# Performance work log

Measured on AMD Instinct MI355X. Metric: run time of the kernel, lower is better.

Reference implementation:

```python
import jax, jax.numpy as jnp
import numpy as np

B, T, D = 2, 2048, 1024
H = 16
HD = D // H  # 64


def setup_inputs() -> dict:
    key = jax.random.key(0)
    k1, k2, k3, k4, k5 = jax.random.split(key, 5)
    s = 0.02
    return {
        "x": jax.random.normal(k1, (B, T, D), dtype=jnp.float32),
        "Wqkv": jax.random.normal(k2, (D, 3 * D), dtype=jnp.float32) * s,
        "bqkv": jax.random.normal(k3, (3 * D,), dtype=jnp.float32) * s,
        "Wout": jax.random.normal(k4, (D, D), dtype=jnp.float32) * s,
        "bout": jax.random.normal(k5, (D,), dtype=jnp.float32) * s,
    }


def reference(x, Wqkv, bqkv, Wout, bout):
    b, t, c = x.shape
    qkv = (x @ Wqkv + bqkv).reshape(b, t, 3, H, HD)
    q = jnp.transpose(qkv[:, :, 0], (0, 2, 1, 3))  # [B,H,T,HD]
    k = jnp.transpose(qkv[:, :, 1], (0, 2, 1, 3))
    v = jnp.transpose(qkv[:, :, 2], (0, 2, 1, 3))
    att = jnp.einsum("bhqd,bhkd->bhqk", q, k) * (HD ** -0.5)
    mask = jnp.tril(jnp.ones((t, t), dtype=bool))  # causal, no past kv
    att = jnp.where(mask, att, -jnp.inf)
    att = jax.nn.softmax(att, axis=-1)
    y = jnp.einsum("bhqk,bhkd->bhqd", att, v)
    y = jnp.transpose(y, (0, 2, 1, 3)).reshape(b, t, c)
    return y @ Wout + bout
```

## Files before the change

### kernel.cpp

```cpp
#include <hip/hip_runtime.h>
#include <hip/hip_bf16.h>
#include <math.h>

#define B_  2
#define T_  2048
#define D_  1024
#define H_  16
#define HD_ 64

typedef __attribute__((ext_vector_type(8))) short short8;
typedef __attribute__((ext_vector_type(4))) float f32x4;

#if __has_builtin(__builtin_amdgcn_exp2f)
#define EXP2F __builtin_amdgcn_exp2f
#else
#define EXP2F exp2f
#endif

__device__ __forceinline__ ushort f2bf(float x) {
    unsigned u = __builtin_bit_cast(unsigned, x);
    return (ushort)((u + 0x7FFFu + ((u >> 16) & 1u)) >> 16);
}

__device__ __forceinline__ unsigned pack_bf2_fast(float a, float b) {
    unsigned ua = __builtin_bit_cast(unsigned, a) + 0x8000u;
    unsigned ub = __builtin_bit_cast(unsigned, b) + 0x8000u;
    return (ua >> 16) | (ub & 0xFFFF0000u);
}

__device__ __forceinline__ void load_lds_16B(const ushort* g, ushort* l) {
    __builtin_amdgcn_global_load_lds(
        (const __attribute__((address_space(1))) unsigned*)g,
        (__attribute__((address_space(3))) unsigned*)l, 16, 0, 0);
}

__global__ __launch_bounds__(256)
void cast_x_kernel(const float* __restrict__ x, ushort* __restrict__ xb, int n4)
{
    int i = blockIdx.x * blockDim.x + threadIdx.x;
    for (; i < n4; i += gridDim.x * blockDim.x) {
        float4 v = ((const float4*)x)[i];
        ushort4 o = { f2bf(v.x), f2bf(v.y), f2bf(v.z), f2bf(v.w) };
        ((ushort4*)xb)[i] = o;
    }
}

__global__ __launch_bounds__(256)
void transpose_cast_w(const float* __restrict__ W, ushort* __restrict__ Wt,
                      int K, int M)
{
    __shared__ ushort Ts[64][65];
    const int m0 = blockIdx.x * 64, k0 = blockIdx.y * 64;
    const int tr = threadIdx.x >> 4;
    const int tc = threadIdx.x & 15;
    #pragma unroll
    for (int it = 0; it < 4; it++) {
        int k = tr + it * 16;
        float4 v = *(const float4*)&W[(size_t)(k0 + k) * M + m0 + tc * 4];
        Ts[tc * 4 + 0][k] = f2bf(v.x);
        Ts[tc * 4 + 1][k] = f2bf(v.y);
        Ts[tc * 4 + 2][k] = f2bf(v.z);
        Ts[tc * 4 + 3][k] = f2bf(v.w);
    }
    __syncthreads();
    const int mr = threadIdx.x >> 2;
    const int c4 = threadIdx.x & 3;
    #pragma unroll
    for (int it = 0; it < 4; it++) {
        int kk = c4 * 16 + it * 4;
        ushort4 o = { Ts[mr][kk], Ts[mr][kk + 1], Ts[mr][kk + 2], Ts[mr][kk + 3] };
        *(ushort4*)&Wt[(size_t)(m0 + mr) * K + k0 + kk] = o;
    }
}

template<int MODE>
__global__ __launch_bounds__(256)
void mfma_gemm(const ushort* __restrict__ A, const ushort* __restrict__ Bt,
               const float* __restrict__ bias, float* __restrict__ C,
               ushort* __restrict__ Qg, ushort* __restrict__ Kg,
               ushort* __restrict__ Vtg, int K, int M)
{
    __shared__ __align__(16) ushort lds[16384];
    ushort* Asl = lds;
    ushort* Bsl = lds + 8192;

    const int tid = threadIdx.x;
    const int w  = tid >> 6, L = tid & 63;
    const int lt = L & 15, lq = L >> 4;
    const int wr = w >> 1, wc = w & 1;
    const int m0 = blockIdx.x * 128, n0 = blockIdx.y * 128;
    const int rsub = L >> 3;
    const int pgr  = L & 7;

    f32x4 acc[4][4] = {};

    for (int k0 = 0; k0 < K; k0 += 64) {
        __syncthreads();
        #pragma unroll
        for (int j = 0; j < 4; j++) {
            const int row  = (w * 4 + j) * 8 + rsub;
            const int gran = pgr ^ rsub;
            load_lds_16B(A  + (size_t)(n0 + row) * K + k0 + gran * 8,
                         &Asl[row * 64 + pgr * 8]);
            load_lds_16B(Bt + (size_t)(m0 + row) * K + k0 + gran * 8,
                         &Bsl[row * 64 + pgr * 8]);
        }
        __syncthreads();

        #pragma unroll
        for (int ks = 0; ks < 2; ks++) {
            short8 af[4], bf[4];
            #pragma unroll
            for (int i = 0; i < 4; i++) {
                const int ra = wr * 64 + i * 16 + lt;
                af[i] = *(const short8*)&Asl[ra * 64 + (((ks * 4 + lq) ^ (ra & 7)) * 8)];
                const int rb = wc * 64 + i * 16 + lt;
                bf[i] = *(const short8*)&Bsl[rb * 64 + (((ks * 4 + lq) ^ (rb & 7)) * 8)];
            }
            #pragma unroll
            for (int i = 0; i < 4; i++)
                #pragma unroll
                for (int j = 0; j < 4; j++)
                    acc[i][j] = __builtin_amdgcn_mfma_f32_16x16x32_bf16(af[i], bf[j], acc[i][j], 0, 0, 0);
        }
    }

    if (MODE == 0) {
        #pragma unroll
        for (int j = 0; j < 4; j++) {
            const int m = m0 + wc * 64 + j * 16 + lt;
            const float bv = bias[m];
            #pragma unroll
            for (int i = 0; i < 4; i++) {
                const int n = n0 + wr * 64 + i * 16 + lq * 4;
                #pragma unroll
                for (int r = 0; r < 4; r++)
                    C[(size_t)(n + r) * M + m] = acc[i][j][r] + bv;
            }
        }
    } else {
        const int s = m0 >> 10;
        const float qs = (s == 0) ? 0.18033688011112042f : 1.0f;
        #pragma unroll
        for (int j = 0; j < 4; j++) {
            const int m = m0 + wc * 64 + j * 16 + lt;
            const float bv = bias[m];
            const int h = (m >> 6) & 15, d = m & 63;
            #pragma unroll
            for (int i = 0; i < 4; i++) {
                const int n = n0 + wr * 64 + i * 16 + lq * 4;
                const int b = n >> 11, t = n & 2047;
                if (s < 2) {
                    ushort* dst = (s == 0 ? Qg : Kg);
                    #pragma unroll
                    for (int r = 0; r < 4; r++)
                        dst[((size_t)(b * H_ + h) * T_ + t + r) * HD_ + d] =
                            f2bf((acc[i][j][r] + bv) * qs);
                } else {
                    ushort4 o = { f2bf(acc[i][j][0] + bv), f2bf(acc[i][j][1] + bv),
                                  f2bf(acc[i][j][2] + bv), f2bf(acc[i][j][3] + bv) };
                    *(ushort4*)&Vtg[((size_t)(b * H_ + h) * HD_ + d) * T_ + t] = o;
                }
            }
        }
    }
}

__global__ __launch_bounds__(256, 4)
void attn_mfma(const ushort* __restrict__ Qg, const ushort* __restrict__ Kg,
               const ushort* __restrict__ Vtg, ushort* __restrict__ yb)
{
    const int h = blockIdx.y, b = blockIdx.z;
    const int flip = ((blockIdx.y >> 3) ^ blockIdx.z) & 1;
    const int qb = flip ? blockIdx.x : (31 - blockIdx.x);
    const int tid = threadIdx.x;
    const int w  = tid >> 6, L = tid & 63;
    const int lt = L & 15, lq = L >> 4;
    const int kswz = lt & 7;

    __shared__ __align__(16) ushort Ks [128 * 64];
    __shared__ __align__(16) ushort Vts[64 * 128];
    __shared__ __align__(16) ushort Ps [4][16 * 40];

    const size_t bh = (size_t)(b * H_ + h);
    const ushort* Qbase  = Qg  + bh * T_ * HD_;
    const ushort* Kbase  = Kg  + bh * T_ * HD_;
    const ushort* Vtbase = Vtg + bh * HD_ * T_;

    const int q_glob = qb * 64 + w * 16 + lt;
    const short8 qf0 = *(const short8*)(Qbase + (size_t)q_glob * HD_ + lq * 8);
    const short8 qf1 = *(const short8*)(Qbase + (size_t)q_glob * HD_ + 32 + lq * 8);

    f32x4 acc_o[4] = {};
    float lsum = 0.f;

    const int krow = tid >> 3, kpg = tid & 7;
    const int vrow = tid >> 4, vpg = tid & 15;
    const int nk = (qb + 2) >> 1;

    for (int kb = 0; kb < nk; kb++) {
        __syncthreads();
        #pragma unroll
        for (int rr = 0; rr < 4; rr++) {
            const int row = krow + 32 * rr;
            load_lds_16B(Kbase + (size_t)(kb * 128 + row) * HD_ + (kpg ^ (row & 7)) * 8,
                         &Ks[row * 64 + kpg * 8]);
        }
        #pragma unroll
        for (int rr = 0; rr < 4; rr++) {
            const int d = vrow + 16 * rr;
            load_lds_16B(Vtbase + (size_t)d * T_ + kb * 128 + (vpg ^ (d & 7)) * 8,
                         &Vts[d * 128 + vpg * 8]);
        }
        __syncthreads();

        if (kb < nk - 1) {
            #pragma unroll
            for (int ks = 0; ks < 4; ks++) {
                const int row0 = (2 * ks) * 16 + lt;
                const int row1 = row0 + 16;
                short8 a00 = *(const short8*)&Ks[row0 * 64 + ((lq ^ kswz) * 8)];
                short8 a01 = *(const short8*)&Ks[row0 * 64 + (((4 + lq) ^ kswz) * 8)];
                short8 a10 = *(const short8*)&Ks[row1 * 64 + ((lq ^ kswz) * 8)];
                short8 a11 = *(const short8*)&Ks[row1 * 64 + (((4 + lq) ^ kswz) * 8)];
                f32x4 c0 = {}, c1 = {};
                c0 = __builtin_amdgcn_mfma_f32_16x16x32_bf16(a00, qf0, c0, 0, 0, 0);
                c0 = __builtin_amdgcn_mfma_f32_16x16x32_bf16(a01, qf1, c0, 0, 0, 0);
                c1 = __builtin_amdgcn_mfma_f32_16x16x32_bf16(a10, qf0, c1, 0, 0, 0);
                c1 = __builtin_amdgcn_mfma_f32_16x16x32_bf16(a11, qf1, c1, 0, 0, 0);

                float p0 = EXP2F(c0[0]), p1 = EXP2F(c0[1]);
                float p2 = EXP2F(c0[2]), p3 = EXP2F(c0[3]);
                float p4 = EXP2F(c1[0]), p5 = EXP2F(c1[1]);
                float p6 = EXP2F(c1[2]), p7 = EXP2F(c1[3]);
                lsum += ((p0 + p1) + (p2 + p3)) + ((p4 + p5) + (p6 + p7));
                uint2 pk0 = { pack_bf2_fast(p0, p1), pack_bf2_fast(p2, p3) };
                uint2 pk1 = { pack_bf2_fast(p4, p5), pack_bf2_fast(p6, p7) };
                *(uint2*)&Ps[w][lt * 40 + lq * 4]      = pk0;
                *(uint2*)&Ps[w][lt * 40 + 16 + lq * 4] = pk1;

                short8 pf = *(const short8*)&Ps[w][lt * 40 + lq * 8];

                #pragma unroll
                for (int dt = 0; dt < 4; dt++) {
                    const int vr = dt * 16 + lt;
                    short8 vf = *(const short8*)&Vts[vr * 128 + (((ks * 4 + lq) ^ kswz) * 8)];
                    acc_o[dt] = __builtin_amdgcn_mfma_f32_16x16x32_bf16(pf, vf, acc_o[dt], 0, 0, 0);
                }
            }
        } else {
            const int ksN = (qb & 1) ? 4 : 2;
            const int mk0 = (qb & 1) ? 2 : 0;
            for (int ks = 0; ks < ksN; ks++) {
                const int row0 = (2 * ks) * 16 + lt;
                const int row1 = row0 + 16;
                short8 a00 = *(const short8*)&Ks[row0 * 64 + ((lq ^ kswz) * 8)];
                short8 a01 = *(const short8*)&Ks[row0 * 64 + (((4 + lq) ^ kswz) * 8)];
                short8 a10 = *(const short8*)&Ks[row1 * 64 + ((lq ^ kswz) * 8)];
                short8 a11 = *(const short8*)&Ks[row1 * 64 + (((4 + lq) ^ kswz) * 8)];
                f32x4 c0 = {}, c1 = {};
                c0 = __builtin_amdgcn_mfma_f32_16x16x32_bf16(a00, qf0, c0, 0, 0, 0);
                c0 = __builtin_amdgcn_mfma_f32_16x16x32_bf16(a01, qf1, c0, 0, 0, 0);
                c1 = __builtin_amdgcn_mfma_f32_16x16x32_bf16(a10, qf0, c1, 0, 0, 0);
                c1 = __builtin_amdgcn_mfma_f32_16x16x32_bf16(a11, qf1, c1, 0, 0, 0);

                float p[8];
                #pragma unroll
                for (int r = 0; r < 4; r++) { p[r] = EXP2F(c0[r]); p[4 + r] = EXP2F(c1[r]); }
                if (ks >= mk0) {
                    const int key0 = kb * 128 + (2 * ks) * 16 + lq * 4;
                    #pragma unroll
                    for (int r = 0; r < 4; r++) {
                        if (key0 + r > q_glob)      p[r] = 0.f;
                        if (key0 + 16 + r > q_glob) p[4 + r] = 0.f;
                    }
                }
                lsum += ((p[0] + p[1]) + (p[2] + p[3])) + ((p[4] + p[5]) + (p[6] + p[7]));
                uint2 pk0 = { pack_bf2_fast(p[0], p[1]), pack_bf2_fast(p[2], p[3]) };
                uint2 pk1 = { pack_bf2_fast(p[4], p[5]), pack_bf2_fast(p[6], p[7]) };
                *(uint2*)&Ps[w][lt * 40 + lq * 4]      = pk0;
                *(uint2*)&Ps[w][lt * 40 + 16 + lq * 4] = pk1;

                short8 pf = *(const short8*)&Ps[w][lt * 40 + lq * 8];

                #pragma unroll
                for (int dt = 0; dt < 4; dt++) {
                    const int vr = dt * 16 + lt;
                    short8 vf = *(const short8*)&Vts[vr * 128 + (((ks * 4 + lq) ^ kswz) * 8)];
                    acc_o[dt] = __builtin_amdgcn_mfma_f32_16x16x32_bf16(pf, vf, acc_o[dt], 0, 0, 0);
                }
            }
        }
    }

    lsum += __shfl_xor(lsum, 16, 64);
    lsum += __shfl_xor(lsum, 32, 64);
    const float inv = 1.0f / lsum;

    float linv[4];
    #pragma unroll
    for (int r = 0; r < 4; r++) linv[r] = __shfl(inv, lq * 4 + r, 64);

    ushort* ybase = yb + (size_t)(b * T_ + qb * 64 + w * 16) * D_ + h * HD_;
    #pragma unroll
    for (int r = 0; r < 4; r++)
        #pragma unroll
        for (int dt = 0; dt < 4; dt++)
            ybase[(size_t)(lq * 4 + r) * D_ + dt * 16 + lt] = f2bf(acc_o[dt][r] * linv[r]);
}

extern "C" void kernel_launch(void* const* d_in, const int* in_sizes, int n_in,
                              void* d_out, int out_size, void* d_ws, size_t ws_size,
                              hipStream_t stream)
{
    const float* x    = (const float*)d_in[0];
    const float* Wqkv = (const float*)d_in[1];
    const float* bqkv = (const float*)d_in[2];
    const float* Wout = (const float*)d_in[3];
    const float* bout = (const float*)d_in[4];
    float* out = (float*)d_out;

    char* ws = (char*)d_ws;
    const size_t NT = (size_t)B_ * T_;
    ushort* xb     = (ushort*)ws;
    ushort* Wqkvt  = (ushort*)(ws + NT * D_ * 2);
    ushort* Woutt  = (ushort*)(ws + NT * D_ * 2 + (size_t)3 * D_ * D_ * 2);
    char*   p      = ws + NT * D_ * 2 + (size_t)4 * D_ * D_ * 2;
    const size_t qkv_elems = (size_t)B_ * H_ * T_ * HD_;
    ushort* Qg  = (ushort*)p;
    ushort* Kg  = (ushort*)(p + qkv_elems * 2);
    ushort* Vtg = (ushort*)(p + qkv_elems * 4);
    ushort* yb  = (ushort*)(p + qkv_elems * 6);

    cast_x_kernel<<<1024, 256, 0, stream>>>(x, xb, (int)(NT * D_ / 4));
    transpose_cast_w<<<dim3(3 * D_ / 64, D_ / 64), 256, 0, stream>>>(Wqkv, Wqkvt, D_, 3 * D_);
    transpose_cast_w<<<dim3(D_ / 64, D_ / 64), 256, 0, stream>>>(Wout, Woutt, D_, D_);

    mfma_gemm<1><<<dim3(3 * D_ / 128, NT / 128), 256, 0, stream>>>(
        xb, Wqkvt, bqkv, nullptr, Qg, Kg, Vtg, D_, 3 * D_);

    attn_mfma<<<dim3(32, H_, B_), 256, 0, stream>>>(Qg, Kg, Vtg, yb);

    mfma_gemm<0><<<dim3(D_ / 128, NT / 128), 256, 0, stream>>>(
        yb, Woutt, bout, out, nullptr, nullptr, nullptr, D_, D_);
}
```

Before: 180.2 us.

## Load attention K/V fragments directly from global and narrow out-projection GEMM tile

The attention kernel stops staging K and V^T tiles in shared memory behind block-wide barriers. Each wave now reads its MFMA operand fragments straight from global memory (relying on L2/cache reuse), and the main and last key blocks are merged into one loop with a masked tail. Separately, the GEMM is templated on its N tile width, and the output projection uses 64-wide tiles to double its block count for better CU occupancy. The risks are uncoalesced, redundant global loads per wave in attention, and less data reuse per block in the smaller GEMM tile.

```diff
diff --git a/kernel.cpp b/kernel.cpp
--- a/kernel.cpp
+++ b/kernel.cpp
@@ -73,14 +73,15 @@
     }
 }
 
-template<int MODE>
+template<int MODE, int BN>
 __global__ __launch_bounds__(256)
 void mfma_gemm(const ushort* __restrict__ A, const ushort* __restrict__ Bt,
                const float* __restrict__ bias, float* __restrict__ C,
                ushort* __restrict__ Qg, ushort* __restrict__ Kg,
                ushort* __restrict__ Vtg, int K, int M)
 {
-    __shared__ __align__(16) ushort lds[16384];
+    constexpr int JT = BN / 64;
+    __shared__ __align__(16) ushort lds[8192 + BN * 64];
     ushort* Asl = lds;
     ushort* Bsl = lds + 8192;
 
@@ -88,11 +89,11 @@
     const int w  = tid >> 6, L = tid & 63;
     const int lt = L & 15, lq = L >> 4;
     const int wr = w >> 1, wc = w & 1;
-    const int m0 = blockIdx.x * 128, n0 = blockIdx.y * 128;
+    const int m0 = blockIdx.x * BN, n0 = blockIdx.y * 128;
     const int rsub = L >> 3;
     const int pgr  = L & 7;
 
-    f32x4 acc[4][4] = {};
+    f32x4 acc[4][2 * JT] = {};
 
     for (int k0 = 0; k0 < K; k0 += 64) {
         __syncthreads();
@@ -100,8 +101,13 @@
         for (int j = 0; j < 4; j++) {
             const int row  = (w * 4 + j) * 8 + rsub;
             const int gran = pgr ^ rsub;
-            load_lds_16B(A  + (size_t)(n0 + row) * K + k0 + gran * 8,
+            load_lds_16B(A + (size_t)(n0 + row) * K + k0 + gran * 8,
                          &Asl[row * 64 + pgr * 8]);
+        }
+        #pragma unroll
+        for (int j = 0; j < BN / 32; j++) {
+            const int row  = (w * (BN / 32) + j) * 8 + rsub;
+            const int gran = pgr ^ rsub;
             load_lds_16B(Bt + (size_t)(m0 + row) * K + k0 + gran * 8,
                          &Bsl[row * 64 + pgr * 8]);
         }
@@ -109,26 +115,29 @@
 
         #pragma unroll
         for (int ks = 0; ks < 2; ks++) {
-            short8 af[4], bf[4];
+            short8 af[4], bf[2 * JT];
             #pragma unroll
             for (int i = 0; i < 4; i++) {
                 const int ra = wr * 64 + i * 16 + lt;
                 af[i] = *(const short8*)&Asl[ra * 64 + (((ks * 4 + lq) ^ (ra & 7)) * 8)];
-                const int rb = wc * 64 + i * 16 + lt;
-                bf[i] = *(const short8*)&Bsl[rb * 64 + (((ks * 4 + lq) ^ (rb & 7)) * 8)];
+            }
+            #pragma unroll
+            for (int j = 0; j < 2 * JT; j++) {
+                const int rb = wc * (BN / 2) + j * 16 + lt;
+                bf[j] = *(const short8*)&Bsl[rb * 64 + (((ks * 4 + lq) ^ (rb & 7)) * 8)];
             }
             #pragma unroll
             for (int i = 0; i < 4; i++)
                 #pragma unroll
-                for (int j = 0; j < 4; j++)
+                for (int j = 0; j < 2 * JT; j++)
                     acc[i][j] = __builtin_amdgcn_mfma_f32_16x16x32_bf16(af[i], bf[j], acc[i][j], 0, 0, 0);
         }
     }
 
     if (MODE == 0) {
         #pragma unroll
-        for (int j = 0; j < 4; j++) {
-            const int m = m0 + wc * 64 + j * 16 + lt;
+        for (int j = 0; j < 2 * JT; j++) {
+            const int m = m0 + wc * (BN / 2) + j * 16 + lt;
             const float bv = bias[m];
             #pragma unroll
             for (int i = 0; i < 4; i++) {
@@ -142,8 +151,8 @@
         const int s = m0 >> 10;
         const float qs = (s == 0) ? 0.18033688011112042f : 1.0f;
         #pragma unroll
-        for (int j = 0; j < 4; j++) {
-            const int m = m0 + wc * 64 + j * 16 + lt;
+        for (int j = 0; j < 2 * JT; j++) {
+            const int m = m0 + wc * (BN / 2) + j * 16 + lt;
             const float bv = bias[m];
             const int h = (m >> 6) & 15, d = m & 63;
             #pragma unroll
@@ -176,16 +185,13 @@
     const int tid = threadIdx.x;
     const int w  = tid >> 6, L = tid & 63;
     const int lt = L & 15, lq = L >> 4;
-    const int kswz = lt & 7;
-
-    __shared__ __align__(16) ushort Ks [128 * 64];
-    __shared__ __align__(16) ushort Vts[64 * 128];
-    __shared__ __align__(16) ushort Ps [4][16 * 40];
+
+    __shared__ __align__(16) ushort Ps[4][16 * 40];
 
     const size_t bh = (size_t)(b * H_ + h);
     const ushort* Qbase  = Qg  + bh * T_ * HD_;
-    const ushort* Kbase  = Kg  + bh * T_ * HD_;
-    const ushort* Vtbase = Vtg + bh * HD_ * T_;
+    const ushort* Kf     = Kg  + bh * T_ * HD_ + (size_t)lt * HD_ + lq * 8;
+    const ushort* Vf     = Vtg + bh * HD_ * T_ + (size_t)lt * T_  + lq * 8;
 
     const int q_glob = qb * 64 + w * 16 + lt;
     const short8 qf0 = *(const short8*)(Qbase + (size_t)q_glob * HD_ + lq * 8);
@@ -193,103 +199,55 @@
 
     f32x4 acc_o[4] = {};
     float lsum = 0.f;
-
-    const int krow = tid >> 3, kpg = tid & 7;
-    const int vrow = tid >> 4, vpg = tid & 15;
     const int nk = (qb + 2) >> 1;
 
     for (int kb = 0; kb < nk; kb++) {
-        __syncthreads();
-        #pragma unroll
-        for (int rr = 0; rr < 4; rr++) {
-            const int row = krow + 32 * rr;
-            load_lds_16B(Kbase + (size_t)(kb * 128 + row) * HD_ + (kpg ^ (row & 7)) * 8,
-                         &Ks[row * 64 + kpg * 8]);
-        }
-        #pragma unroll
-        for (int rr = 0; rr < 4; rr++) {
-            const int d = vrow + 16 * rr;
-            load_lds_16B(Vtbase + (size_t)d * T_ + kb * 128 + (vpg ^ (d & 7)) * 8,
-                         &Vts[d * 128 + vpg * 8]);
-        }
-        __syncthreads();
-
-        if (kb < nk - 1) {
-            #pragma unroll
-            for (int ks = 0; ks < 4; ks++) {
-                const int row0 = (2 * ks) * 16 + lt;
-                const int row1 = row0 + 16;
-                short8 a00 = *(const short8*)&Ks[row0 * 64 + ((lq ^ kswz) * 8)];
-                short8 a01 = *(const short8*)&Ks[row0 * 64 + (((4 + lq) ^ kswz) * 8)];
-                short8 a10 = *(const short8*)&Ks[row1 * 64 + ((lq ^ kswz) * 8)];
-                short8 a11 = *(const short8*)&Ks[row1 * 64 + (((4 + lq) ^ kswz) * 8)];
-                f32x4 c0 = {}, c1 = {};
-                c0 = __builtin_amdgcn_mfma_f32_16x16x32_bf16(a00, qf0, c0, 0, 0, 0);
-                c0 = __builtin_amdgcn_mfma_f32_16x16x32_bf16(a01, qf1, c0, 0, 0, 0);
-                c1 = __builtin_amdgcn_mfma_f32_16x16x32_bf16(a10, qf0, c1, 0, 0, 0);
-                c1 = __builtin_amdgcn_mfma_f32_16x16x32_bf16(a11, qf1, c1, 0, 0, 0);
-
-                float p0 = EXP2F(c0[0]), p1 = EXP2F(c0[1]);
-                float p2 = EXP2F(c0[2]), p3 = EXP2F(c0[3]);
-                float p4 = EXP2F(c1[0]), p5 = EXP2F(c1[1]);
-                float p6 = EXP2F(c1[2]), p7 = EXP2F(c1[3]);
-                lsum += ((p0 + p1) + (p2 + p3)) + ((p4 + p5) + (p6 + p7));
-                uint2 pk0 = { pack_bf2_fast(p0, p1), pack_bf2_fast(p2, p3) };
-                uint2 pk1 = { pack_bf2_fast(p4, p5), pack_bf2_fast(p6, p7) };
-                *(uint2*)&Ps[w][lt * 40 + lq * 4]      = pk0;
-                *(uint2*)&Ps[w][lt * 40 + 16 + lq * 4] = pk1;
-
-                short8 pf = *(const short8*)&Ps[w][lt * 40 + lq * 8];
-
+        const bool last = (kb == nk - 1);
+        const int ksN = (!last || (qb & 1)) ? 4 : 2;
+        const int mk0 = last ? ((qb & 1) ? 2 : 0) : 4;
+
+        for (int ks = 0; ks < ksN; ks++) {
+            const int key0 = kb * 128 + ks * 32;
+            const ushort* kp = Kf + (size_t)key0 * HD_;
+            short8 a00 = *(const short8*)(kp);
+            short8 a01 = *(const short8*)(kp + 32);
+            short8 a10 = *(const short8*)(kp + 16 * HD_);
+            short8 a11 = *(const short8*)(kp + 16 * HD_ + 32);
+            const ushort* vp = Vf + key0;
+            short8 vf0 = *(const short8*)(vp);
+            short8 vf1 = *(const short8*)(vp + 16 * T_);
+            short8 vf2 = *(const short8*)(vp + 32 * T_);
+            short8 vf3 = *(const short8*)(vp + 48 * T_);
+
+            f32x4 c0 = {}, c1 = {};
+            c0 = __builtin_amdgcn_mfma_f32_16x16x32_bf16(a00, qf0, c0, 0, 0, 0);
+            c0 = __builtin_amdgcn_mfma_f32_16x16x32_bf16(a01, qf1, c0, 0, 0, 0);
+            c1 = __builtin_amdgcn_mfma_f32_16x16x32_bf16(a10, qf0, c1, 0, 0, 0);
+            c1 = __builtin_amdgcn_mfma_f32_16x16x32_bf16(a11, qf1, c1, 0, 0, 0);
+
+            float p[8];
+            #pragma unroll
+            for (int r = 0; r < 4; r++) { p[r] = EXP2F(c0[r]); p[4 + r] = EXP2F(c1[r]); }
+            if (ks >= mk0) {
+                const int kq = key0 + lq * 4;
                 #pragma unroll
-                for (int dt = 0; dt < 4; dt++) {
-                    const int vr = dt * 16 + lt;
-                    short8 vf = *(const short8*)&Vts[vr * 128 + (((ks * 4 + lq) ^ kswz) * 8)];
-                    acc_o[dt] = __builtin_amdgcn_mfma_f32_16x16x32_bf16(pf, vf, acc_o[dt], 0, 0, 0);
+                for (int r = 0; r < 4; r++) {
+                    if (kq + r > q_glob)      p[r] = 0.f;
+                    if (kq + 16 + r > q_glob) p[4 + r] = 0.f;
                 }
             }
-        } else {
-            const int ksN = (qb & 1) ? 4 : 2;
-            const int mk0 = (qb & 1) ? 2 : 0;
-            for (int ks = 0; ks < ksN; ks++) {
-                const int row0 = (2 * ks) * 16 + lt;
-                const int row1 = row0 + 16;
-                short8 a00 = *(const short8*)&Ks[row0 * 64 + ((lq ^ kswz) * 8)];
-                short8 a01 = *(const short8*)&Ks[row0 * 64 + (((4 + lq) ^ kswz) * 8)];
-                short8 a10 = *(const short8*)&Ks[row1 * 64 + ((lq ^ kswz) * 8)];
-                short8 a11 = *(const short8*)&Ks[row1 * 64 + (((4 + lq) ^ kswz) * 8)];
-                f32x4 c0 = {}, c1 = {};
-                c0 = __builtin_amdgcn_mfma_f32_16x16x32_bf16(a00, qf0, c0, 0, 0, 0);
-                c0 = __builtin_amdgcn_mfma_f32_16x16x32_bf16(a01, qf1, c0, 0, 0, 0);
-                c1 = __builtin_amdgcn_mfma_f32_16x16x32_bf16(a10, qf0, c1, 0, 0, 0);
-                c1 = __builtin_amdgcn_mfma_f32_16x16x32_bf16(a11, qf1, c1, 0, 0, 0);
-
-                float p[8];
-                #pragma unroll
-                for (int r = 0; r < 4; r++) { p[r] = EXP2F(c0[r]); p[4 + r] = EXP2F(c1[r]); }
-                if (ks >= mk0) {
-                    const int key0 = kb * 128 + (2 * ks) * 16 + lq * 4;
-                    #pragma unroll
-                    for (int r = 0; r < 4; r++) {
-                        if (key0 + r > q_glob)      p[r] = 0.f;
-                        if (key0 + 16 + r > q_glob) p[4 + r] = 0.f;
-                    }
-                }
-                lsum += ((p[0] + p[1]) + (p[2] + p[3])) + ((p[4] + p[5]) + (p[6] + p[7]));
-                uint2 pk0 = { pack_bf2_fast(p[0], p[1]), pack_bf2_fast(p[2], p[3]) };
-                uint2 pk1 = { pack_bf2_fast(p[4], p[5]), pack_bf2_fast(p[6], p[7]) };
-                *(uint2*)&Ps[w][lt * 40 + lq * 4]      = pk0;
-                *(uint2*)&Ps[w][lt * 40 + 16 + lq * 4] = pk1;
-
-                short8 pf = *(const short8*)&Ps[w][lt * 40 + lq * 8];
-
-                #pragma unroll
-                for (int dt = 0; dt < 4; dt++) {
-                    const int vr = dt * 16 + lt;
-                    short8 vf = *(const short8*)&Vts[vr * 128 + (((ks * 4 + lq) ^ kswz) * 8)];
-                    acc_o[dt] = __builtin_amdgcn_mfma_f32_16x16x32_bf16(pf, vf, acc_o[dt], 0, 0, 0);
-                }
-            }
+            lsum += ((p[0] + p[1]) + (p[2] + p[3])) + ((p[4] + p[5]) + (p[6] + p[7]));
+            uint2 pk0 = { pack_bf2_fast(p[0], p[1]), pack_bf2_fast(p[2], p[3]) };
+            uint2 pk1 = { pack_bf2_fast(p[4], p[5]), pack_bf2_fast(p[6], p[7]) };
+            *(uint2*)&Ps[w][lt * 40 + lq * 4]      = pk0;
+            *(uint2*)&Ps[w][lt * 40 + 16 + lq * 4] = pk1;
+
+            short8 pf = *(const short8*)&Ps[w][lt * 40 + lq * 8];
+
+            acc_o[0] = __builtin_amdgcn_mfma_f32_16x16x32_bf16(pf, vf0, acc_o[0], 0, 0, 0);
+            acc_o[1] = __builtin_amdgcn_mfma_f32_16x16x32_bf16(pf, vf1, acc_o[1], 0, 0, 0);
+            acc_o[2] = __builtin_amdgcn_mfma_f32_16x16x32_bf16(pf, vf2, acc_o[2], 0, 0, 0);
+            acc_o[3] = __builtin_amdgcn_mfma_f32_16x16x32_bf16(pf, vf3, acc_o[3], 0, 0, 0);
         }
     }
 
@@ -336,11 +294,11 @@
     transpose_cast_w<<<dim3(3 * D_ / 64, D_ / 64), 256, 0, stream>>>(Wqkv, Wqkvt, D_, 3 * D_);
     transpose_cast_w<<<dim3(D_ / 64, D_ / 64), 256, 0, stream>>>(Wout, Woutt, D_, D_);
 
-    mfma_gemm<1><<<dim3(3 * D_ / 128, NT / 128), 256, 0, stream>>>(
+    mfma_gemm<1, 128><<<dim3(3 * D_ / 128, NT / 128), 256, 0, stream>>>(
         xb, Wqkvt, bqkv, nullptr, Qg, Kg, Vtg, D_, 3 * D_);
 
     attn_mfma<<<dim3(32, H_, B_), 256, 0, stream>>>(Qg, Kg, Vtg, yb);
 
-    mfma_gemm<0><<<dim3(D_ / 128, NT / 128), 256, 0, stream>>>(
+    mfma_gemm<0, 64><<<dim3(D_ / 64, NT / 128), 256, 0, stream>>>(
         yb, Woutt, bout, out, nullptr, nullptr, nullptr, D_, D_);
 }
```

Result: slower. 259.7 us (+44.1%).
